# Performance work log

Measured on AMD Instinct MI355X. Metric: run time of the kernel, lower is better.

Reference implementation:

```python
import jax, jax.numpy as jnp
import numpy as np

B, IN, E, HID, OUT = 16384, 256, 32, 64, 128


def setup_inputs() -> dict:
    key = jax.random.key(0)
    ks = jax.random.split(key, 14)
    s = 0.05
    return {
        "x": jax.random.normal(ks[0], (B, IN), dtype=jnp.float32),
        "Wg": jax.random.normal(ks[1], (IN, E), dtype=jnp.float32) * s,
        "bg": jnp.zeros((E,), dtype=jnp.float32),
        "W1": jax.random.normal(ks[2], (E, IN, HID), dtype=jnp.float32) * s,
        "b1": jnp.zeros((E, HID), dtype=jnp.float32),
        "W2": jax.random.normal(ks[3], (E, HID, 256), dtype=jnp.float32) * s,
        "b2": jnp.zeros((E, 256), dtype=jnp.float32),
        "W3": jax.random.normal(ks[4], (E, 256, 128), dtype=jnp.float32) * s,
        "b3": jnp.zeros((E, 128), dtype=jnp.float32),
        "W4": jax.random.normal(ks[5], (E, 128, HID), dtype=jnp.float32) * s,
        "b4": jnp.zeros((E, HID), dtype=jnp.float32),
        "W5": jax.random.normal(ks[6], (E, HID, OUT), dtype=jnp.float32) * s,
        "b5": jnp.zeros((E, OUT), dtype=jnp.float32),
    }


def reference(x, Wg, bg, W1, b1, W2, b2, W3, b3, W4, b4, W5, b5):
    # Gating: softmax over experts. [B, E]
    g = jax.nn.softmax(x @ Wg + bg, axis=1)
    # All experts evaluated densely via batched GEMMs (fused expert axis).
    h = jax.nn.relu(jnp.einsum('bi,eih->beh', x, W1) + b1)   # [B,E,64]
    h = jax.nn.relu(jnp.einsum('beh,ehm->bem', h, W2) + b2)  # [B,E,256]
    # Dropout(0.2) is identity in eval mode.
    h = jax.nn.relu(jnp.einsum('bem,emn->ben', h, W3) + b3)  # [B,E,128]
    h = jax.nn.relu(jnp.einsum('ben,enh->beh', h, W4) + b4)  # [B,E,64]
    y = jnp.einsum('beh,eho->beo', h, W5) + b5               # [B,E,OUT]
    # Gating-weighted sum over experts: einsum('bi,bij->bj').
    return jnp.einsum('be,beo->bo', g, y)
```

## Files before the change

kernel.cpp:

```cpp
#include <hip/hip_runtime.h>

#define BB      16384
#define IN_DIM  256
#define NE      32
#define H1D     64
#define H2D     256
#define H3D     128
#define NOUT    128

typedef __bf16 bf16_t;
typedef __bf16 bf16x4_t __attribute__((ext_vector_type(4)));
typedef __bf16 bf16x8  __attribute__((ext_vector_type(8)));
typedef float  f32x4   __attribute__((ext_vector_type(4)));

#define OFF_WF   ((size_t)0)
#define OFF_WGF  ((size_t)NE * 81920 * 2)

__global__ __launch_bounds__(256) void build_frags(
    const float* __restrict__ W1, const float* __restrict__ W2,
    const float* __restrict__ W3, const float* __restrict__ W4,
    const float* __restrict__ W5, const float* __restrict__ Wg,
    bf16_t* __restrict__ Wf, bf16_t* __restrict__ Wgf)
{
    const int g    = blockIdx.x * 256 + threadIdx.x;
    const int lane = g & 63;
    const int set  = g >> 6;
    const float* src; bf16_t* dst; int N, t, ks;
    if (set < 5120) {
        const int e = set / 160;
        const int s = set % 160;
        dst = Wf + (size_t)e * 81920 + ((size_t)s * 64 + lane) * 8;
        if (s < 32)       { t = s >> 3;         ks = s & 7;         N = 64;  src = W1 + (size_t)e * 16384; }
        else if (s < 64)  { t = (s - 32) >> 1;  ks = (s - 32) & 1;  N = 256; src = W2 + (size_t)e * 16384; }
        else if (s < 128) { t = (s - 64) >> 3;  ks = (s - 64) & 7;  N = 128; src = W3 + (size_t)e * 32768; }
        else if (s < 144) { t = (s - 128) >> 2; ks = (s - 128) & 3; N = 64;  src = W4 + (size_t)e * 8192;  }
        else              { t = (s - 144) >> 1; ks = (s - 144) & 1; N = 128; src = W5 + (size_t)e * 8192;  }
    } else {
        const int s = set - 5120;
        t = s >> 3; ks = s & 7; N = 32; src = Wg;
        dst = Wgf + ((size_t)s * 64 + lane) * 8;
    }
    const int f  = t * 16 + (lane & 15);
    const int k0 = ks * 32 + (lane >> 4) * 8;
    bf16x8 o;
#pragma unroll
    for (int j = 0; j < 8; j++) o[j] = (bf16_t)src[(size_t)(k0 + j) * N + f];
    *(bf16x8*)dst = o;
}

template<int RS>
__device__ __forceinline__ void* swzp(char* base, int row, int byteoff) {
    const int g = byteoff >> 4;
    return (void*)(base + ((row << RS) | ((g ^ (row & 7)) << 4) | (byteoff & 15)));
}

#define L_H1   0
#define L_SX   8192
#define L_H2   40960
#define L_H3   73728
#define L_H4   90112
#define L_SG   98304
#define L_TOT  106496

__global__ __launch_bounds__(512) void moe_main(
    const float* __restrict__ x, const bf16_t* __restrict__ Wf,
    const bf16_t* __restrict__ Wgf, const float* __restrict__ bg,
    const float* __restrict__ b1, const float* __restrict__ b2,
    const float* __restrict__ b3, const float* __restrict__ b4,
    const float* __restrict__ b5, float* __restrict__ out)
{
    __shared__ __align__(16) char lds[L_TOT];
    char* sX = lds + L_SX;
    char* h1 = lds + L_H1;
    char* h2 = lds + L_H2;
    char* h3 = lds + L_H3;
    char* h4 = lds + L_H4;
    float* sG = (float*)(lds + L_SG);

    const int tid  = threadIdx.x;
    const int w    = tid >> 6;
    const int lane = tid & 63;
    const int c    = lane & 15;
    const int q    = lane >> 4;
    const int fg   = w & 3;
    const int mh   = w >> 2;
    const int b0   = blockIdx.x * 64;

    bf16x8 wA[8], wB[2][2], wD[4], wE[2];

#pragma unroll
    for (int ks = 0; ks < 8; ks++)
        wA[ks] = *(const bf16x8*)(Wf + ((size_t)(fg * 8 + ks) * 64 + lane) * 8);
#pragma unroll
    for (int nt = 0; nt < 2; nt++)
#pragma unroll
        for (int ks = 0; ks < 2; ks++)
            wB[nt][ks] = *(const bf16x8*)(Wf + 16384 + ((size_t)((w * 2 + nt) * 2 + ks) * 64 + lane) * 8);

    {
        const int r  = tid >> 3;
        const int c0 = (tid & 7) * 32;
        const float* sp = x + (size_t)(b0 + r) * IN_DIM + c0;
#pragma unroll
        for (int jj = 0; jj < 4; jj++) {
            const float4 v0 = *(const float4*)(sp + jj * 8);
            const float4 v1 = *(const float4*)(sp + jj * 8 + 4);
            bf16x8 o = { (bf16_t)v0.x, (bf16_t)v0.y, (bf16_t)v0.z, (bf16_t)v0.w,
                         (bf16_t)v1.x, (bf16_t)v1.y, (bf16_t)v1.z, (bf16_t)v1.w };
            *(bf16x8*)swzp<9>(sX, r, c0 * 2 + jj * 16) = o;
        }
    }
    __syncthreads();

    {
        const int t = w & 1, m = w >> 1;
        f32x4 acc = (f32x4){0.f, 0.f, 0.f, 0.f};
#pragma unroll
        for (int ks = 0; ks < 8; ks++) {
            bf16x8 xv = *(const bf16x8*)swzp<9>(sX, m * 16 + c, ks * 64 + q * 16);
            bf16x8 wg = *(const bf16x8*)(Wgf + ((size_t)(t * 8 + ks) * 64 + lane) * 8);
            acc = __builtin_amdgcn_mfma_f32_16x16x32_bf16(wg, xv, acc, 0, 0, 0);
        }
        const float4 bgv = *(const float4*)(bg + t * 16 + q * 4);
        float* sLgF = (float*)h3;
        *(float4*)(sLgF + (size_t)(m * 16 + c) * 36 + t * 16 + q * 4) =
            (float4){acc[0] + bgv.x, acc[1] + bgv.y, acc[2] + bgv.z, acc[3] + bgv.w};
    }
    __syncthreads();

    {
        const int r = tid >> 3;
        const int j = tid & 7;
        const float* sLgF = (const float*)h3;
        float4 l = *(const float4*)(sLgF + (size_t)r * 36 + j * 4);
        float mx = fmaxf(fmaxf(l.x, l.y), fmaxf(l.z, l.w));
#pragma unroll
        for (int off = 1; off < 8; off <<= 1) mx = fmaxf(mx, __shfl_xor(mx, off));
        float e0 = __expf(l.x - mx), e1 = __expf(l.y - mx),
              e2 = __expf(l.z - mx), e3 = __expf(l.w - mx);
        float sm = e0 + e1 + e2 + e3;
#pragma unroll
        for (int off = 1; off < 8; off <<= 1) sm += __shfl_xor(sm, off);
        const float rs = 1.f / sm;
        sG[(j * 4 + 0) * 64 + r] = e0 * rs;
        sG[(j * 4 + 1) * 64 + r] = e1 * rs;
        sG[(j * 4 + 2) * 64 + r] = e2 * rs;
        sG[(j * 4 + 3) * 64 + r] = e3 * rs;
    }
    {
        const float4 bv = *(const float4*)(b1 + fg * 16 + q * 4);
#pragma unroll
        for (int mm = 0; mm < 2; mm++) {
            const int m = mh * 2 + mm;
            f32x4 acc = (f32x4){0.f, 0.f, 0.f, 0.f};
#pragma unroll
            for (int ks = 0; ks < 8; ks++) {
                bf16x8 xv = *(const bf16x8*)swzp<9>(sX, m * 16 + c, ks * 64 + q * 16);
                acc = __builtin_amdgcn_mfma_f32_16x16x32_bf16(wA[ks], xv, acc, 0, 0, 0);
            }
            bf16x4_t hv = { (bf16_t)fmaxf(acc[0] + bv.x, 0.f),
                            (bf16_t)fmaxf(acc[1] + bv.y, 0.f),
                            (bf16_t)fmaxf(acc[2] + bv.z, 0.f),
                            (bf16_t)fmaxf(acc[3] + bv.w, 0.f) };
            *(bf16x4_t*)swzp<7>(h1, m * 16 + c, fg * 32 + q * 8) = hv;
        }
    }
    __syncthreads();

    float oacc[4][4];
#pragma unroll
    for (int m = 0; m < 4; m++)
#pragma unroll
        for (int r = 0; r < 4; r++) oacc[m][r] = 0.f;

    auto do_l5 = [&](int ep) {
        const float4 bv = *(const float4*)(b5 + (size_t)ep * NOUT + w * 16 + q * 4);
#pragma unroll
        for (int m = 0; m < 4; m++) {
            f32x4 acc = (f32x4){0.f, 0.f, 0.f, 0.f};
#pragma unroll
            for (int ks = 0; ks < 2; ks++) {
                bf16x8 ha = *(const bf16x8*)swzp<7>(h4, m * 16 + c, ks * 64 + q * 16);
                acc = __builtin_amdgcn_mfma_f32_16x16x32_bf16(wE[ks], ha, acc, 0, 0, 0);
            }
            const float gv = sG[ep * 64 + m * 16 + c];
            oacc[m][0] += gv * (acc[0] + bv.x);
            oacc[m][1] += gv * (acc[1] + bv.y);
            oacc[m][2] += gv * (acc[2] + bv.z);
            oacc[m][3] += gv * (acc[3] + bv.w);
        }
    };

    auto do_l4 = [&](int ep) {
        const float4 bv = *(const float4*)(b4 + (size_t)ep * H1D + fg * 16 + q * 4);
#pragma unroll
        for (int mm = 0; mm < 2; mm++) {
            const int m = mh * 2 + mm;
            f32x4 acc = (f32x4){0.f, 0.f, 0.f, 0.f};
#pragma unroll
            for (int ks = 0; ks < 4; ks++) {
                bf16x8 ha = *(const bf16x8*)swzp<8>(h3, m * 16 + c, ks * 64 + q * 16);
                acc = __builtin_amdgcn_mfma_f32_16x16x32_bf16(wD[ks], ha, acc, 0, 0, 0);
            }
            bf16x4_t hv = { (bf16_t)fmaxf(acc[0] + bv.x, 0.f),
                            (bf16_t)fmaxf(acc[1] + bv.y, 0.f),
                            (bf16_t)fmaxf(acc[2] + bv.z, 0.f),
                            (bf16_t)fmaxf(acc[3] + bv.w, 0.f) };
            *(bf16x4_t*)swzp<7>(h4, m * 16 + c, fg * 32 + q * 8) = hv;
        }
    };

    for (int e = 0; e < NE; e++) {
        const bf16_t* We  = Wf + (size_t)e * 81920;
        const bf16_t* Wen = Wf + (size_t)((e + 1) & 31) * 81920;
        const bf16_t* Wep = Wf + (size_t)((e - 1) & 31) * 81920;

#pragma unroll
        for (int ks = 0; ks < 8; ks++)
            wA[ks] = *(const bf16x8*)(Wen + ((size_t)(fg * 8 + ks) * 64 + lane) * 8);
#pragma unroll
        for (int ks = 0; ks < 2; ks++)
            wE[ks] = *(const bf16x8*)(Wep + 73728 + ((size_t)(w * 2 + ks) * 64 + lane) * 8);

        {
            float4 bv[2];
#pragma unroll
            for (int nt = 0; nt < 2; nt++)
                bv[nt] = *(const float4*)(b2 + (size_t)e * H2D + (w * 2 + nt) * 16 + q * 4);
#pragma unroll
            for (int m = 0; m < 4; m++) {
                bf16x8 ha[2];
#pragma unroll
                for (int ks = 0; ks < 2; ks++)
                    ha[ks] = *(const bf16x8*)swzp<7>(h1, m * 16 + c, ks * 64 + q * 16);
                f32x4 acc[2];
#pragma unroll
                for (int nt = 0; nt < 2; nt++) acc[nt] = (f32x4){0.f, 0.f, 0.f, 0.f};
#pragma unroll
                for (int nt = 0; nt < 2; nt++)
#pragma unroll
                    for (int ks = 0; ks < 2; ks++)
                        acc[nt] = __builtin_amdgcn_mfma_f32_16x16x32_bf16(wB[nt][ks], ha[ks], acc[nt], 0, 0, 0);
#pragma unroll
                for (int nt = 0; nt < 2; nt++) {
                    bf16x4_t hv = { (bf16_t)fmaxf(acc[nt][0] + bv[nt].x, 0.f),
                                    (bf16_t)fmaxf(acc[nt][1] + bv[nt].y, 0.f),
                                    (bf16_t)fmaxf(acc[nt][2] + bv[nt].z, 0.f),
                                    (bf16_t)fmaxf(acc[nt][3] + bv[nt].w, 0.f) };
                    *(bf16x4_t*)swzp<9>(h2, m * 16 + c, (w * 2 + nt) * 32 + q * 8) = hv;
                }
            }
        }
        if (e > 0) do_l4(e - 1);
        __syncthreads();

        bf16x8 wC[2][8];
#pragma unroll
        for (int jt = 0; jt < 2; jt++)
#pragma unroll
            for (int ks = 0; ks < 8; ks++)
                wC[jt][ks] = *(const bf16x8*)(We + 32768 + ((size_t)((fg * 2 + jt) * 8 + ks) * 64 + lane) * 8);
#pragma unroll
        for (int nt = 0; nt < 2; nt++)
#pragma unroll
            for (int ks = 0; ks < 2; ks++)
                wB[nt][ks] = *(const bf16x8*)(Wen + 16384 + ((size_t)((w * 2 + nt) * 2 + ks) * 64 + lane) * 8);
#pragma unroll
        for (int ks = 0; ks < 4; ks++)
            wD[ks] = *(const bf16x8*)(We + 65536 + ((size_t)(fg * 4 + ks) * 64 + lane) * 8);

        {
            float4 bv[2];
#pragma unroll
            for (int jt = 0; jt < 2; jt++)
                bv[jt] = *(const float4*)(b3 + (size_t)e * H3D + (fg * 2 + jt) * 16 + q * 4);
#pragma unroll
            for (int mm = 0; mm < 2; mm++) {
                const int m = mh * 2 + mm;
                f32x4 acc[2];
#pragma unroll
                for (int jt = 0; jt < 2; jt++) acc[jt] = (f32x4){0.f, 0.f, 0.f, 0.f};
#pragma unroll
                for (int ks = 0; ks < 8; ks++) {
                    bf16x8 ha = *(const bf16x8*)swzp<9>(h2, m * 16 + c, ks * 64 + q * 16);
#pragma unroll
                    for (int jt = 0; jt < 2; jt++)
                        acc[jt] = __builtin_amdgcn_mfma_f32_16x16x32_bf16(wC[jt][ks], ha, acc[jt], 0, 0, 0);
                }
#pragma unroll
                for (int jt = 0; jt < 2; jt++) {
                    bf16x4_t hv = { (bf16_t)fmaxf(acc[jt][0] + bv[jt].x, 0.f),
                                    (bf16_t)fmaxf(acc[jt][1] + bv[jt].y, 0.f),
                                    (bf16_t)fmaxf(acc[jt][2] + bv[jt].z, 0.f),
                                    (bf16_t)fmaxf(acc[jt][3] + bv[jt].w, 0.f) };
                    *(bf16x4_t*)swzp<8>(h3, m * 16 + c, (fg * 2 + jt) * 32 + q * 8) = hv;
                }
            }
        }
        if (e < NE - 1) {
            const float4 bv = *(const float4*)(b1 + (size_t)(e + 1) * H1D + fg * 16 + q * 4);
#pragma unroll
            for (int mm = 0; mm < 2; mm++) {
                const int m = mh * 2 + mm;
                f32x4 acc = (f32x4){0.f, 0.f, 0.f, 0.f};
#pragma unroll
                for (int ks = 0; ks < 8; ks++) {
                    bf16x8 xv = *(const bf16x8*)swzp<9>(sX, m * 16 + c, ks * 64 + q * 16);
                    acc = __builtin_amdgcn_mfma_f32_16x16x32_bf16(wA[ks], xv, acc, 0, 0, 0);
                }
                bf16x4_t hv = { (bf16_t)fmaxf(acc[0] + bv.x, 0.f),
                                (bf16_t)fmaxf(acc[1] + bv.y, 0.f),
                                (bf16_t)fmaxf(acc[2] + bv.z, 0.f),
                                (bf16_t)fmaxf(acc[3] + bv.w, 0.f) };
                *(bf16x4_t*)swzp<7>(h1, m * 16 + c, fg * 32 + q * 8) = hv;
            }
        }
        if (e > 0) do_l5(e - 1);
        __syncthreads();
    }

    do_l4(NE - 1);
#pragma unroll
    for (int ks = 0; ks < 2; ks++)
        wE[ks] = *(const bf16x8*)(Wf + (size_t)31 * 81920 + 73728 + ((size_t)(w * 2 + ks) * 64 + lane) * 8);
    __syncthreads();
    do_l5(NE - 1);

#pragma unroll
    for (int m = 0; m < 4; m++)
        *(float4*)(out + (size_t)(b0 + m * 16 + c) * NOUT + w * 16 + q * 4) =
            (float4){oacc[m][0], oacc[m][1], oacc[m][2], oacc[m][3]};
}

extern "C" void kernel_launch(void* const* d_in, const int* in_sizes, int n_in,
                              void* d_out, int out_size, void* d_ws, size_t ws_size,
                              hipStream_t stream)
{
    (void)in_sizes; (void)n_in; (void)out_size; (void)ws_size;
    const float* x  = (const float*)d_in[0];
    const float* Wg = (const float*)d_in[1];
    const float* bg = (const float*)d_in[2];
    const float* W1 = (const float*)d_in[3];
    const float* b1 = (const float*)d_in[4];
    const float* W2 = (const float*)d_in[5];
    const float* b2 = (const float*)d_in[6];
    const float* W3 = (const float*)d_in[7];
    const float* b3 = (const float*)d_in[8];
    const float* W4 = (const float*)d_in[9];
    const float* b4 = (const float*)d_in[10];
    const float* W5 = (const float*)d_in[11];
    const float* b5 = (const float*)d_in[12];

    char* ws = (char*)d_ws;
    bf16_t* Wf  = (bf16_t*)(ws + OFF_WF);
    bf16_t* Wgf = (bf16_t*)(ws + OFF_WGF);
    float*  outp = (float*)d_out;

    build_frags<<<dim3(1284), dim3(256), 0, stream>>>(W1, W2, W3, W4, W5, Wg, Wf, Wgf);
    moe_main<<<dim3(BB / 64), dim3(512), 0, stream>>>(x, Wf, Wgf, bg,
                                                      b1, b2, b3, b4, b5, outp);
}
```

Before: 249.9 us.

## Repartition layer-3 work per wave and prefetch W3 fragments earlier

Layer 3 work is split differently across waves. Before, each wave computed two output column tiles for half the rows. Now each wave owns one 16-column tile across all four row tiles, which halves the per-wave W3 fragment registers (8 instead of 16). The W3 fragment load moves to the top of the expert loop, before layer 2, so its latency hides behind layer-2 compute, and the W5 prefetch moves after the barrier. The cost is more LDS reads of h2 per wave (four row tiles instead of two) and a different register pressure balance.

```diff
diff --git a/kernel.cpp b/kernel.cpp
--- a/kernel.cpp
+++ b/kernel.cpp
@@ -86,7 +86,7 @@
     const int mh   = w >> 2;
     const int b0   = blockIdx.x * 64;
 
-    bf16x8 wA[8], wB[2][2], wD[4], wE[2];
+    bf16x8 wA[8], wB[2][2], wC[8], wD[4], wE[2];
 
 #pragma unroll
     for (int ks = 0; ks < 8; ks++)
@@ -217,10 +217,10 @@
 
 #pragma unroll
         for (int ks = 0; ks < 8; ks++)
+            wC[ks] = *(const bf16x8*)(We + 32768 + ((size_t)(w * 8 + ks) * 64 + lane) * 8);
+#pragma unroll
+        for (int ks = 0; ks < 8; ks++)
             wA[ks] = *(const bf16x8*)(Wen + ((size_t)(fg * 8 + ks) * 64 + lane) * 8);
-#pragma unroll
-        for (int ks = 0; ks < 2; ks++)
-            wE[ks] = *(const bf16x8*)(Wep + 73728 + ((size_t)(w * 2 + ks) * 64 + lane) * 8);
 
         {
             float4 bv[2];
@@ -254,12 +254,11 @@
         if (e > 0) do_l4(e - 1);
         __syncthreads();
 
-        bf16x8 wC[2][8];
-#pragma unroll
-        for (int jt = 0; jt < 2; jt++)
-#pragma unroll
-            for (int ks = 0; ks < 8; ks++)
-                wC[jt][ks] = *(const bf16x8*)(We + 32768 + ((size_t)((fg * 2 + jt) * 8 + ks) * 64 + lane) * 8);
+        if (e > 0) {
+#pragma unroll
+            for (int ks = 0; ks < 2; ks++)
+                wE[ks] = *(const bf16x8*)(Wep + 73728 + ((size_t)(w * 2 + ks) * 64 + lane) * 8);
+        }
 #pragma unroll
         for (int nt = 0; nt < 2; nt++)
 #pragma unroll
@@ -270,31 +269,20 @@
             wD[ks] = *(const bf16x8*)(We + 65536 + ((size_t)(fg * 4 + ks) * 64 + lane) * 8);
 
         {
-            float4 bv[2];
-#pragma unroll
-            for (int jt = 0; jt < 2; jt++)
-                bv[jt] = *(const float4*)(b3 + (size_t)e * H3D + (fg * 2 + jt) * 16 + q * 4);
-#pragma unroll
-            for (int mm = 0; mm < 2; mm++) {
-                const int m = mh * 2 + mm;
-                f32x4 acc[2];
-#pragma unroll
-                for (int jt = 0; jt < 2; jt++) acc[jt] = (f32x4){0.f, 0.f, 0.f, 0.f};
+            const float4 bv = *(const float4*)(b3 + (size_t)e * H3D + w * 16 + q * 4);
+#pragma unroll
+            for (int m = 0; m < 4; m++) {
+                f32x4 acc = (f32x4){0.f, 0.f, 0.f, 0.f};
 #pragma unroll
                 for (int ks = 0; ks < 8; ks++) {
                     bf16x8 ha = *(const bf16x8*)swzp<9>(h2, m * 16 + c, ks * 64 + q * 16);
-#pragma unroll
-                    for (int jt = 0; jt < 2; jt++)
-                        acc[jt] = __builtin_amdgcn_mfma_f32_16x16x32_bf16(wC[jt][ks], ha, acc[jt], 0, 0, 0);
+                    acc = __builtin_amdgcn_mfma_f32_16x16x32_bf16(wC[ks], ha, acc, 0, 0, 0);
                 }
-#pragma unroll
-                for (int jt = 0; jt < 2; jt++) {
-                    bf16x4_t hv = { (bf16_t)fmaxf(acc[jt][0] + bv[jt].x, 0.f),
-                                    (bf16_t)fmaxf(acc[jt][1] + bv[jt].y, 0.f),
-                                    (bf16_t)fmaxf(acc[jt][2] + bv[jt].z, 0.f),
-                                    (bf16_t)fmaxf(acc[jt][3] + bv[jt].w, 0.f) };
-                    *(bf16x4_t*)swzp<8>(h3, m * 16 + c, (fg * 2 + jt) * 32 + q * 8) = hv;
-                }
+                bf16x4_t hv = { (bf16_t)fmaxf(acc[0] + bv.x, 0.f),
+                                (bf16_t)fmaxf(acc[1] + bv.y, 0.f),
+                                (bf16_t)fmaxf(acc[2] + bv.z, 0.f),
+                                (bf16_t)fmaxf(acc[3] + bv.w, 0.f) };
+                *(bf16x4_t*)swzp<8>(h3, m * 16 + c, w * 32 + q * 8) = hv;
             }
         }
         if (e < NE - 1) {
@@ -319,10 +307,10 @@
         __syncthreads();
     }
 
-    do_l4(NE - 1);
 #pragma unroll
     for (int ks = 0; ks < 2; ks++)
         wE[ks] = *(const bf16x8*)(Wf + (size_t)31 * 81920 + 73728 + ((size_t)(w * 2 + ks) * 64 + lane) * 8);
+    do_l4(NE - 1);
     __syncthreads();
     do_l5(NE - 1);
 
```

New measurement: 226.3 us. 1.1x faster.
